# Kernel optimization log

Hardware: AMD Instinct MI355X
Metric: run time of the kernel (lower is better)

Reference implementation:

```python
import jax, jax.numpy as jnp
import numpy as np

# dims
BB, T, D_IN = 16, 2048, 64
D = 512          # hidden_dim (d_model)
DI = 2 * D       # d_inner (expand=2)
N = 16           # d_state
DC = 4           # d_conv
R = D // 16      # dt_rank = 32
L = 3            # n_layer
D_OUT = 128


def setup_inputs() -> dict:
    key = jax.random.key(0)
    ks = jax.random.split(key, 10)
    g = lambda k, shape, s: (jax.random.normal(k, shape, jnp.float32) * s)
    A_log = jnp.tile(jnp.log(jnp.arange(1, N + 1, dtype=jnp.float32))[None, None, :], (L, DI, 1))
    return {
        "x": g(ks[0], (BB, T, D_IN), 1.0),
        "Wi": g(ks[1], (D, D_IN), 0.05), "bi": jnp.zeros((D,), jnp.float32),
        "Win": g(ks[2], (L, 2 * DI, D), 0.02),
        "convw": g(ks[3], (L, DI, DC), 0.2), "convb": jnp.zeros((L, DI), jnp.float32),
        "Wx": g(ks[4], (L, R + 2 * N, DI), 0.02),
        "Wdt": g(ks[5], (L, DI, R), 0.05), "bdt": jnp.full((L, DI), -1.0, jnp.float32),
        "A_log": A_log, "Dp": jnp.ones((L, DI), jnp.float32),
        "Wout": g(ks[6], (L, D, DI), 0.02),
        "Wo": g(ks[7], (D_OUT, D), 0.05), "bo": jnp.zeros((D_OUT,), jnp.float32),
    }


def _selective_scan(u, delta, A, Bm, Cm, Dv):
    # u, delta: [B,T,DI]; A: [DI,N]; Bm, Cm: [B,T,N]; Dv: [DI]
    def step(h, inp):
        d_t, u_t, B_t, C_t = inp  # [B,DI],[B,DI],[B,N],[B,N]
        dA = jnp.exp(d_t[:, :, None] * A)                      # [B,DI,N]
        h = dA * h + (d_t * u_t)[:, :, None] * B_t[:, None, :]  # [B,DI,N]
        y = jnp.einsum('bdn,bn->bd', h, C_t)
        return h, y

    h0 = jnp.zeros((u.shape[0], u.shape[2], A.shape[1]), u.dtype)
    xs = (delta.transpose(1, 0, 2), u.transpose(1, 0, 2),
          Bm.transpose(1, 0, 2), Cm.transpose(1, 0, 2))
    _, ys = jax.lax.scan(step, h0, xs)
    return ys.transpose(1, 0, 2) + u * Dv


def _mamba_layer(x, Win, cw, cb, Wx, Wdt, bdt, A_log, Dv, Wout):
    xz = x @ Win.T                      # [B,T,2*DI]
    xin, z = jnp.split(xz, 2, axis=-1)
    # causal depthwise conv1d
    xc = jax.lax.conv_general_dilated(
        xin.transpose(0, 2, 1), cw[:, None, :], (1,), [(DC - 1, 0)],
        feature_group_count=DI, dimension_numbers=('NCH', 'OIH', 'NCH'))
    u = jax.nn.silu((xc + cb[None, :, None]).transpose(0, 2, 1))  # [B,T,DI]
    dbc = u @ Wx.T                      # [B,T,R+2N]
    dt, Bm, Cm = dbc[..., :R], dbc[..., R:R + N], dbc[..., R + N:]
    delta = jax.nn.softplus(dt @ Wdt.T + bdt)
    A = -jnp.exp(A_log)
    y = _selective_scan(u, delta, A, Bm, Cm, Dv)
    return (y * jax.nn.silu(z)) @ Wout.T


def reference(x, Wi, bi, Win, convw, convb, Wx, Wdt, bdt, A_log, Dp, Wout, Wo, bo):
    h = x @ Wi.T + bi
    for l in range(L):
        h = _mamba_layer(h, Win[l], convw[l], convb[l], Wx[l], Wdt[l], bdt[l],
                         A_log[l], Dp[l], Wout[l])
    return jnp.tanh(h @ Wo.T + bo)  # [B,T,output_dim]
```

## Files before the change

### kernel.cpp

```cpp
#include <hip/hip_runtime.h>
#include <hip/hip_bf16.h>

#define BB_ 16
#define T_ 2048
#define DIN_ 64
#define D_ 512
#define DI_ 1024
#define N_ 16
#define DC_ 4
#define R_ 32
#define L_ 3
#define DOUT_ 128
#define CL_ 64
#define NCH_ (T_ / CL_)

typedef __attribute__((ext_vector_type(8))) _Float16 f16x8;
typedef __attribute__((ext_vector_type(4))) float f32x4;

__device__ __forceinline__ float silu_f(float x) { return x / (1.f + __expf(-x)); }

__device__ __forceinline__ float softplus_f(float t) {
    return fmaxf(t, 0.f) + __logf(1.f + __expf(-fabsf(t)));
}

__device__ __forceinline__ unsigned short f2h(float f) {
    union { _Float16 h; unsigned short u; } c;
    c.h = (_Float16)f;
    return c.u;
}

__device__ __forceinline__ float h2f(unsigned short u) {
    union { unsigned short u; _Float16 h; } c;
    c.u = u;
    return (float)c.h;
}

__device__ __forceinline__ void gload_lds16(const unsigned short* g,
                                            unsigned short* l) {
    __builtin_amdgcn_global_load_lds(
        (const __attribute__((address_space(1))) void*)g,
        (__attribute__((address_space(3))) void*)l, 16, 0, 0);
}

__device__ __forceinline__ float decode_scale(unsigned int bits) {
    if (bits == 0u) return 1.f;
    const int E = (int)(bits >> 23) & 0xFF;
    return __uint_as_float((unsigned)(265 - E) << 23);
}

__device__ __forceinline__ uint4 pack8(float4 lo, float4 hi, float s) {
    union { uint4 u; unsigned short h[8]; } r;
    r.h[0] = f2h(lo.x * s); r.h[1] = f2h(lo.y * s);
    r.h[2] = f2h(lo.z * s); r.h[3] = f2h(lo.w * s);
    r.h[4] = f2h(hi.x * s); r.h[5] = f2h(hi.y * s);
    r.h[6] = f2h(hi.z * s); r.h[7] = f2h(hi.w * s);
    return r.u;
}

__device__ __forceinline__ const float* wregion(
    int r, const float* Win, const float* Wout, const float* Wx,
    const float* Wo, size_t* n4)
{
    if (r < 3)       { *n4 = 262144; return Win  + (size_t)r * 1048576; }
    else if (r < 6)  { *n4 = 131072; return Wout + (size_t)(r - 3) * 524288; }
    else if (r == 6) { *n4 = 16384;  return Wo; }
    else             { *n4 = 16384;  return Wx  + (size_t)(r - 7) * 65536; }
}

__global__ __launch_bounds__(256) void amax_all(
    const float* __restrict__ Win, const float* __restrict__ Wout,
    const float* __restrict__ Wx, const float* __restrict__ Wo,
    unsigned int* __restrict__ scales)
{
    size_t n4;
    const float* p = wregion(blockIdx.z, Win, Wout, Wx, Wo, &n4);
    float m = 0.f;
    for (size_t i = (size_t)blockIdx.x * 256 + threadIdx.x; i < n4;
         i += (size_t)gridDim.x * 256) {
        const float4 v = ((const float4*)p)[i];
        m = fmaxf(m, fmaxf(fmaxf(fabsf(v.x), fabsf(v.y)),
                           fmaxf(fabsf(v.z), fabsf(v.w))));
    }
#pragma unroll
    for (int off = 32; off; off >>= 1) m = fmaxf(m, __shfl_down(m, off));
    __shared__ float sm[4];
    if ((threadIdx.x & 63) == 0) sm[threadIdx.x >> 6] = m;
    __syncthreads();
    if (threadIdx.x == 0) {
        const float b = fmaxf(fmaxf(sm[0], sm[1]), fmaxf(sm[2], sm[3]));
        atomicMax(scales + blockIdx.z, __float_as_uint(b));
    }
}

__global__ __launch_bounds__(256) void cast_all(
    const float* __restrict__ Win, const float* __restrict__ Wout,
    const float* __restrict__ Wx, const float* __restrict__ Wo,
    unsigned short* __restrict__ WinH, unsigned short* __restrict__ WoutH,
    unsigned short* __restrict__ WxH, unsigned short* __restrict__ WoH,
    const unsigned int* __restrict__ scales)
{
    const int r = blockIdx.z;
    size_t n4;
    const float* p = wregion(r, Win, Wout, Wx, Wo, &n4);
    unsigned short* o;
    if (r < 3)       o = WinH  + (size_t)r * 1048576;
    else if (r < 6)  o = WoutH + (size_t)(r - 3) * 524288;
    else if (r == 6) o = WoH;
    else             o = WxH   + (size_t)(r - 7) * 65536;
    const float s = decode_scale(scales[r]);
    for (size_t i = (size_t)blockIdx.x * 256 + threadIdx.x; i < n4;
         i += (size_t)gridDim.x * 256) {
        const float4 v = ((const float4*)p)[i];
        ((ushort4*)o)[i] = make_ushort4(f2h(v.x * s), f2h(v.y * s),
                                        f2h(v.z * s), f2h(v.w * s));
    }
}

__global__ __launch_bounds__(256) void winrow_kernel(
    const float* __restrict__ Win, unsigned int* __restrict__ scales)
{
    const int l = blockIdx.z;
    const int row = blockIdx.x * 4 + (threadIdx.x >> 6);
    const int lane = threadIdx.x & 63;
    const float* W = Win + (size_t)l * 2 * DI_ * D_ + (size_t)row * D_ + lane * 8;
    float s = 0.f;
#pragma unroll
    for (int k = 0; k < 8; k += 4) {
        const float4 v = *(const float4*)(W + k);
        s += fabsf(v.x) + fabsf(v.y) + fabsf(v.z) + fabsf(v.w);
    }
#pragma unroll
    for (int off = 32; off; off >>= 1) s += __shfl_down(s, off);
    if (lane == 0) atomicMax(scales + 26 + l, __float_as_uint(s));
}

__global__ __launch_bounds__(256) void ubound_kernel(
    const float* __restrict__ cw, const float* __restrict__ cb,
    const unsigned int* __restrict__ hslot,
    const unsigned int* __restrict__ wbslot,
    unsigned int* __restrict__ xzbslot, unsigned int* __restrict__ uslot)
{
    const float xzb = __uint_as_float(*hslot) * __uint_as_float(*wbslot);
    if (threadIdx.x == 0) atomicMax(xzbslot, __float_as_uint(xzb));
    float m = 0.f;
    for (int c = threadIdx.x; c < DI_; c += 256) {
        const float4 w = *(const float4*)(cw + (size_t)c * 4);
        const float sw = fabsf(w.x) + fabsf(w.y) + fabsf(w.z) + fabsf(w.w);
        m = fmaxf(m, fabsf(cb[c]) + sw * xzb);
    }
#pragma unroll
    for (int off = 32; off; off >>= 1) m = fmaxf(m, __shfl_down(m, off));
    __shared__ float sm[4];
    if ((threadIdx.x & 63) == 0) sm[threadIdx.x >> 6] = m;
    __syncthreads();
    if (threadIdx.x == 0) {
        const float b = fmaxf(fmaxf(sm[0], sm[1]), fmaxf(sm[2], sm[3]));
        atomicMax(uslot, __float_as_uint(b));
    }
}

template<int ACT, int OUTH>
__global__ __launch_bounds__(256) void gemm_f32a_t128(
    const float* __restrict__ A, int lda,
    const unsigned short* __restrict__ B, int ldb,
    const float* __restrict__ bias,
    void* __restrict__ Cv, int ldc, int K,
    const unsigned int* __restrict__ sa, const unsigned int* __restrict__ sb,
    const unsigned int* __restrict__ so, unsigned int* __restrict__ oamax)
{
    __shared__ __align__(16) unsigned short As[128 * 32];
    __shared__ __align__(16) unsigned short Bs[2][128 * 32];
    const int tid  = threadIdx.x;
    const int lane = tid & 63;
    const int w    = tid >> 6;
    const int wr   = (w >> 1) << 6;
    const int wc   = (w & 1) << 6;
    const int l15  = lane & 15, l4 = lane >> 4;
    const int row0 = blockIdx.y << 7, col0 = blockIdx.x << 7;
    const int tq   = tid >> 2;
    const int tr   = (tid & 3) << 3;

    const float sA  = decode_scale(*sa);
    const float inv = (1.f / sA) * (1.f / decode_scale(*sb));
    const float sOut = OUTH ? decode_scale(*so) : 1.f;

    const float* Ar0 = A + (size_t)(row0 + tq) * lda + tr;
    const float* Ar1 = A + (size_t)(row0 + 64 + tq) * lda + tr;
    const unsigned short* Br0 = B + (size_t)(col0 + tq) * ldb + tr;
    const unsigned short* Br1 = B + (size_t)(col0 + 64 + tq) * ldb + tr;

    f32x4 acc[4][4];
#pragma unroll
    for (int m = 0; m < 4; ++m)
#pragma unroll
        for (int n = 0; n < 4; ++n) acc[m][n] = (f32x4){0.f, 0.f, 0.f, 0.f};

    float4 a0lo = *(const float4*)(Ar0), a0hi = *(const float4*)(Ar0 + 4);
    float4 a1lo = *(const float4*)(Ar1), a1hi = *(const float4*)(Ar1 + 4);
    gload_lds16(Br0, &Bs[0][tq * 32 + tr]);
    gload_lds16(Br1, &Bs[0][(64 + tq) * 32 + tr]);

    int cur = 0;
    for (int k0 = 0; k0 < K; k0 += 32) {
        __syncthreads();
        *(uint4*)&As[tq * 32 + tr]        = pack8(a0lo, a0hi, sA);
        *(uint4*)&As[(64 + tq) * 32 + tr] = pack8(a1lo, a1hi, sA);
        __syncthreads();

        if (k0 + 32 < K) {
            gload_lds16(Br0 + k0 + 32, &Bs[cur ^ 1][tq * 32 + tr]);
            gload_lds16(Br1 + k0 + 32, &Bs[cur ^ 1][(64 + tq) * 32 + tr]);
            a0lo = *(const float4*)(Ar0 + k0 + 32);
            a0hi = *(const float4*)(Ar0 + k0 + 36);
            a1lo = *(const float4*)(Ar1 + k0 + 32);
            a1hi = *(const float4*)(Ar1 + k0 + 36);
        }

        f16x8 af[4], bfr[4];
#pragma unroll
        for (int m = 0; m < 4; ++m)
            af[m] = *(const f16x8*)&As[(wr + m * 16 + l15) * 32 + l4 * 8];
#pragma unroll
        for (int n = 0; n < 4; ++n)
            bfr[n] = *(const f16x8*)&Bs[cur][(wc + n * 16 + l15) * 32 + l4 * 8];
#pragma unroll
        for (int m = 0; m < 4; ++m)
#pragma unroll
            for (int n = 0; n < 4; ++n)
                acc[m][n] = __builtin_amdgcn_mfma_f32_16x16x32_f16(
                    af[m], bfr[n], acc[m][n], 0, 0, 0);
        cur ^= 1;
    }

    float am = 0.f;
#pragma unroll
    for (int n = 0; n < 4; ++n) {
        const int col = col0 + wc + n * 16 + l15;
        float bc = 0.f;
        if (ACT == 3) bc = bias[col];
#pragma unroll
        for (int m = 0; m < 4; ++m) {
            const int rowb = row0 + wr + m * 16 + (l4 << 2);
#pragma unroll
            for (int r = 0; r < 4; ++r) {
                float v = acc[m][n][r] * inv;
                if (ACT == 3) v = tanhf(v + bc);
                if (OUTH) {
                    ((unsigned short*)Cv)[(size_t)(rowb + r) * ldc + col] =
                        f2h(v * sOut);
                } else {
                    ((float*)Cv)[(size_t)(rowb + r) * ldc + col] = v;
                    am = fmaxf(am, fabsf(v));
                }
            }
        }
    }
    if (!OUTH && oamax) {
#pragma unroll
        for (int off = 32; off; off >>= 1) am = fmaxf(am, __shfl_down(am, off));
        if (lane == 0) atomicMax(oamax, __float_as_uint(am));
    }
}

__global__ __launch_bounds__(256) void gemm_f16_t64n(
    const unsigned short* __restrict__ A, int lda,
    const unsigned short* __restrict__ B, int ldb,
    float* __restrict__ C, int ldc, int K,
    const unsigned int* __restrict__ sa, const unsigned int* __restrict__ sb)
{
    __shared__ __align__(16) unsigned short As[128 * 32];
    __shared__ __align__(16) unsigned short Bs[64 * 32];
    const int tid  = threadIdx.x;
    const int lane = tid & 63;
    const int w    = tid >> 6;
    const int l15  = lane & 15, l4 = lane >> 4;
    const int row0 = blockIdx.y << 7;
    const int tq   = tid >> 2;
    const int tr   = (tid & 3) << 3;

    const float inv = (1.f / decode_scale(*sa)) * (1.f / decode_scale(*sb));

    const unsigned short* Ar0 = A + (size_t)(row0 + tq) * lda + tr;
    const unsigned short* Ar1 = A + (size_t)(row0 + 64 + tq) * lda + tr;
    const unsigned short* Br  = B + (size_t)tq * ldb + tr;

    f32x4 acc[2][4];
#pragma unroll
    for (int m = 0; m < 2; ++m)
#pragma unroll
        for (int n = 0; n < 4; ++n) acc[m][n] = (f32x4){0.f, 0.f, 0.f, 0.f};

    uint4 av0 = *(const uint4*)(Ar0);
    uint4 av1 = *(const uint4*)(Ar1);
    uint4 bv  = *(const uint4*)(Br);

    for (int k0 = 0; k0 < K; k0 += 32) {
        __syncthreads();
        *(uint4*)&As[tq * 32 + tr]        = av0;
        *(uint4*)&As[(64 + tq) * 32 + tr] = av1;
        *(uint4*)&Bs[tq * 32 + tr]        = bv;
        __syncthreads();

        if (k0 + 32 < K) {
            av0 = *(const uint4*)(Ar0 + k0 + 32);
            av1 = *(const uint4*)(Ar1 + k0 + 32);
            bv  = *(const uint4*)(Br  + k0 + 32);
        }

        f16x8 af[2], bfr[4];
#pragma unroll
        for (int m = 0; m < 2; ++m)
            af[m] = *(const f16x8*)&As[(w * 32 + m * 16 + l15) * 32 + l4 * 8];
#pragma unroll
        for (int n = 0; n < 4; ++n)
            bfr[n] = *(const f16x8*)&Bs[(n * 16 + l15) * 32 + l4 * 8];
#pragma unroll
        for (int m = 0; m < 2; ++m)
#pragma unroll
            for (int n = 0; n < 4; ++n)
                acc[m][n] = __builtin_amdgcn_mfma_f32_16x16x32_f16(
                    af[m], bfr[n], acc[m][n], 0, 0, 0);
    }

#pragma unroll
    for (int n = 0; n < 4; ++n) {
        const int col = n * 16 + l15;
#pragma unroll
        for (int m = 0; m < 2; ++m) {
            const int rowb = row0 + w * 32 + m * 16 + (l4 << 2);
#pragma unroll
            for (int r = 0; r < 4; ++r)
                C[(size_t)(rowb + r) * ldc + col] = acc[m][n][r] * inv;
        }
    }
}

__global__ __launch_bounds__(256) void gemm_in(
    const float* __restrict__ A, int lda,
    const float* __restrict__ B, int ldb,
    const float* __restrict__ bias,
    float* __restrict__ C, int ldc, int K,
    unsigned int* __restrict__ oamax)
{
    __shared__ __align__(16) float As[8][128];
    __shared__ __align__(16) float Bs[8][128];
    const int tid  = threadIdx.x;
    const int row0 = blockIdx.y << 7;
    const int col0 = blockIdx.x << 7;
    const int tx = tid & 15, ty = tid >> 4;

    float acc[8][8];
#pragma unroll
    for (int i = 0; i < 8; ++i)
#pragma unroll
        for (int j = 0; j < 8; ++j) acc[i][j] = 0.f;

    const int arow = tid >> 1;
    const int acol = (tid & 1) << 2;
    const float* Ap = A + (size_t)(row0 + arow) * lda + acol;
    const float* Bp = B + (size_t)(col0 + arow) * ldb + acol;

    for (int k0 = 0; k0 < K; k0 += 8) {
        const float4 av = *(const float4*)(Ap + k0);
        const float4 bv = *(const float4*)(Bp + k0);
        __syncthreads();
        As[acol + 0][arow] = av.x; As[acol + 1][arow] = av.y;
        As[acol + 2][arow] = av.z; As[acol + 3][arow] = av.w;
        Bs[acol + 0][arow] = bv.x; Bs[acol + 1][arow] = bv.y;
        Bs[acol + 2][arow] = bv.z; Bs[acol + 3][arow] = bv.w;
        __syncthreads();
#pragma unroll
        for (int k = 0; k < 8; ++k) {
            float a[8], b[8];
            *(float4*)&a[0] = *(const float4*)&As[k][ty << 3];
            *(float4*)&a[4] = *(const float4*)&As[k][(ty << 3) + 4];
            *(float4*)&b[0] = *(const float4*)&Bs[k][tx << 3];
            *(float4*)&b[4] = *(const float4*)&Bs[k][(tx << 3) + 4];
#pragma unroll
            for (int i = 0; i < 8; ++i)
#pragma unroll
                for (int j = 0; j < 8; ++j)
                    acc[i][j] = fmaf(a[i], b[j], acc[i][j]);
        }
    }

    float bv8[8];
#pragma unroll
    for (int j = 0; j < 8; ++j) bv8[j] = bias[col0 + (tx << 3) + j];

    float am = 0.f;
#pragma unroll
    for (int i = 0; i < 8; ++i) {
        float v[8];
#pragma unroll
        for (int j = 0; j < 8; ++j) {
            v[j] = acc[i][j] + bv8[j];
            am = fmaxf(am, fabsf(v[j]));
        }
        float* Cp = C + (size_t)(row0 + (ty << 3) + i) * ldc + col0 + (tx << 3);
        *(float4*)(Cp)     = make_float4(v[0], v[1], v[2], v[3]);
        *(float4*)(Cp + 4) = make_float4(v[4], v[5], v[6], v[7]);
    }
#pragma unroll
    for (int off = 32; off; off >>= 1) am = fmaxf(am, __shfl_down(am, off));
    if ((tid & 63) == 0) atomicMax(oamax, __float_as_uint(am));
}

__global__ __launch_bounds__(256) void conv_silu_kernel(
    const unsigned short* __restrict__ xzh, const float* __restrict__ cw,
    const float* __restrict__ cb, unsigned short* __restrict__ u,
    size_t total4, const unsigned int* __restrict__ xzbslot,
    const unsigned int* __restrict__ uslot)
{
    const float invX = 1.f / decode_scale(*xzbslot);
    const float s = decode_scale(*uslot);
    for (size_t i = (size_t)blockIdx.x * 256 + threadIdx.x; i < total4;
         i += (size_t)gridDim.x * 256) {
        const size_t e = i * 4;
        const int c = (int)(e & (DI_ - 1));
        const size_t m = e >> 10;
        const int t = (int)(m & (T_ - 1));
        const unsigned short* xr = xzh + m * 2048 + c;
        float x[4][4];
#pragma unroll
        for (int k = 0; k < 4; ++k) {
            const int dt = 3 - k;
            if (t >= dt) {
                const ushort4 xv = *(const ushort4*)(xr - (size_t)dt * 2048);
                x[k][0] = h2f(xv.x) * invX; x[k][1] = h2f(xv.y) * invX;
                x[k][2] = h2f(xv.z) * invX; x[k][3] = h2f(xv.w) * invX;
            } else {
                x[k][0] = x[k][1] = x[k][2] = x[k][3] = 0.f;
            }
        }
        const float4 cbv = *(const float4*)(cb + c);
        ushort4 o;
        {
            const float4 w = *(const float4*)(cw + (size_t)c * 4);
            o.x = f2h(silu_f(fmaf(x[3][0], w.w, fmaf(x[2][0], w.z,
                     fmaf(x[1][0], w.y, fmaf(x[0][0], w.x, cbv.x))))) * s);
        }
        {
            const float4 w = *(const float4*)(cw + (size_t)(c + 1) * 4);
            o.y = f2h(silu_f(fmaf(x[3][1], w.w, fmaf(x[2][1], w.z,
                     fmaf(x[1][1], w.y, fmaf(x[0][1], w.x, cbv.y))))) * s);
        }
        {
            const float4 w = *(const float4*)(cw + (size_t)(c + 2) * 4);
            o.z = f2h(silu_f(fmaf(x[3][2], w.w, fmaf(x[2][2], w.z,
                     fmaf(x[1][2], w.y, fmaf(x[0][2], w.x, cbv.z))))) * s);
        }
        {
            const float4 w = *(const float4*)(cw + (size_t)(c + 3) * 4);
            o.w = f2h(silu_f(fmaf(x[3][3], w.w, fmaf(x[2][3], w.z,
                     fmaf(x[1][3], w.y, fmaf(x[0][3], w.x, cbv.w))))) * s);
        }
        *(ushort4*)(u + e) = o;
    }
}


__device__ __forceinline__ bool geo_check(const float* a2) {
    bool ok = true;
#pragma unroll
    for (int n = 1; n < N_; ++n)
        ok = ok && (fabsf(a2[n] - a2[0] * (n + 1)) <=
                    1e-5f * fmaxf(1.f, fabsf(a2[n])));
    return ok;
}

__global__ __launch_bounds__(256) void scan_pass1(
    const unsigned short* __restrict__ u, const float* __restrict__ dbc,
    const float* __restrict__ A_log_l, const float* __restrict__ Wdt_l,
    const float* __restrict__ bdt_l, const unsigned int* __restrict__ uslot,
    float* __restrict__ SDL, float* __restrict__ S)
{
    __shared__ __align__(16) float sAll[CL_][64];
    const int tid = threadIdx.x;
    const int b = blockIdx.x, ch = blockIdx.z;
    const int d = (blockIdx.y << 8) + tid;

    float a2[N_], hs[N_];
#pragma unroll
    for (int n = 0; n < N_; ++n) {
        a2[n] = -__expf(A_log_l[d * N_ + n]) * 1.44269504f;
        hs[n] = 0.f;
    }
    const bool geo = geo_check(a2);
    const float invU = 1.f / decode_scale(*uslot);
    float wdt[32];
#pragma unroll
    for (int k = 0; k < 32; k += 4)
        *(float4*)&wdt[k] = *(const float4*)(Wdt_l + (size_t)d * 32 + k);
    const float bdt_d = bdt_l[d];

    const size_t base64 = ((size_t)b * T_ + (size_t)ch * CL_) * 64;
    float* sflat = &sAll[0][0];
    for (int i = tid; i < CL_ * 64; i += 256) sflat[i] = dbc[base64 + i];
    __syncthreads();

    float sdl = 0.f;
    if (geo) {
        for (int tt = 0; tt < CL_; ++tt) {
            float t = bdt_d;
#pragma unroll
            for (int k = 0; k < 32; k += 4) {
                const float4 dv = *(const float4*)&sAll[tt][k];
                t = fmaf(dv.x, wdt[k + 0], t);
                t = fmaf(dv.y, wdt[k + 1], t);
                t = fmaf(dv.z, wdt[k + 2], t);
                t = fmaf(dv.w, wdt[k + 3], t);
            }
            const float dl = softplus_f(t);
            sdl += dl;
            const size_t m = (size_t)b * T_ + ch * CL_ + tt;
            const float du = dl * (h2f(u[m * DI_ + d]) * invU);
            const float r = exp2f(dl * a2[0]);
            float dA = r;
#pragma unroll
            for (int n = 0; n < N_; ++n) {
                hs[n] = fmaf(dA, hs[n], du * sAll[tt][32 + n]);
                dA *= r;
            }
        }
    } else {
        for (int tt = 0; tt < CL_; ++tt) {
            float t = bdt_d;
#pragma unroll
            for (int k = 0; k < 32; k += 4) {
                const float4 dv = *(const float4*)&sAll[tt][k];
                t = fmaf(dv.x, wdt[k + 0], t);
                t = fmaf(dv.y, wdt[k + 1], t);
                t = fmaf(dv.z, wdt[k + 2], t);
                t = fmaf(dv.w, wdt[k + 3], t);
            }
            const float dl = softplus_f(t);
            sdl += dl;
            const size_t m = (size_t)b * T_ + ch * CL_ + tt;
            const float du = dl * (h2f(u[m * DI_ + d]) * invU);
#pragma unroll
            for (int n = 0; n < N_; ++n) {
                const float dA = exp2f(dl * a2[n]);
                hs[n] = fmaf(dA, hs[n], du * sAll[tt][32 + n]);
            }
        }
    }
    SDL[(size_t)((b * NCH_ + ch) << 10) + d] = sdl;
#pragma unroll
    for (int n = 0; n < N_; ++n) {
        const size_t idx = (size_t)(((b * NCH_ + ch) * N_ + n) << 10) + d;
        S[idx] = hs[n];
    }
}

__global__ __launch_bounds__(256) void scan_carry(
    const float* __restrict__ SDL, float* __restrict__ S,
    const float* __restrict__ A_log_l)
{
    const size_t gid = (size_t)blockIdx.x * 256 + threadIdx.x;
    const int d = (int)(gid & 1023);
    const int n = (int)((gid >> 10) & 15);
    const int b = (int)(gid >> 14);
    const float a2n = -__expf(A_log_l[d * N_ + n]) * 1.44269504f;
    float hc = 0.f;
    for (int ch = 0; ch < NCH_; ++ch) {
        const float sdl = SDL[(size_t)((b * NCH_ + ch) << 10) + d];
        const float p = exp2f(sdl * a2n);
        const size_t idx = (size_t)(((b * NCH_ + ch) * N_ + n) << 10) + d;
        const float s = S[idx];
        S[idx] = hc;
        hc = fmaf(p, hc, s);
    }
}

__global__ __launch_bounds__(256) void scan_pass3(
    const unsigned short* __restrict__ xzh, float* __restrict__ g,
    const unsigned short* __restrict__ u, const float* __restrict__ dbc,
    const float* __restrict__ A_log_l, const float* __restrict__ Wdt_l,
    const float* __restrict__ bdt_l, const float* __restrict__ Dp_l,
    const unsigned int* __restrict__ xzbslot,
    const unsigned int* __restrict__ uslot,
    const float* __restrict__ S, unsigned int* __restrict__ gmax)
{
    __shared__ __align__(16) float sAll[CL_][64];
    const int tid = threadIdx.x;
    const int b = blockIdx.x, ch = blockIdx.z;
    const int d = (blockIdx.y << 8) + tid;

    float a2[N_], hs[N_];
#pragma unroll
    for (int n = 0; n < N_; ++n) {
        a2[n] = -__expf(A_log_l[d * N_ + n]) * 1.44269504f;
        hs[n] = S[(size_t)(((b * NCH_ + ch) * N_ + n) << 10) + d];
    }
    const bool geo = geo_check(a2);
    const float invX = 1.f / decode_scale(*xzbslot);
    const float invU = 1.f / decode_scale(*uslot);
    float wdt[32];
#pragma unroll
    for (int k = 0; k < 32; k += 4)
        *(float4*)&wdt[k] = *(const float4*)(Wdt_l + (size_t)d * 32 + k);
    const float bdt_d = bdt_l[d];
    const float Dpd = Dp_l[d];

    const size_t base64 = ((size_t)b * T_ + (size_t)ch * CL_) * 64;
    float* sflat = &sAll[0][0];
    for (int i = tid; i < CL_ * 64; i += 256) sflat[i] = dbc[base64 + i];
    __syncthreads();

    float gm = 0.f;
    if (geo) {
        for (int tt = 0; tt < CL_; ++tt) {
            float t = bdt_d;
#pragma unroll
            for (int k = 0; k < 32; k += 4) {
                const float4 dv = *(const float4*)&sAll[tt][k];
                t = fmaf(dv.x, wdt[k + 0], t);
                t = fmaf(dv.y, wdt[k + 1], t);
                t = fmaf(dv.z, wdt[k + 2], t);
                t = fmaf(dv.w, wdt[k + 3], t);
            }
            const float dl = softplus_f(t);
            const size_t m = (size_t)b * T_ + ch * CL_ + tt;
            const float uv = h2f(u[m * DI_ + d]) * invU;
            const float du = dl * uv;
            const float r = exp2f(dl * a2[0]);
            float dA = r;
            float yv = 0.f;
#pragma unroll
            for (int n = 0; n < N_; ++n) {
                hs[n] = fmaf(dA, hs[n], du * sAll[tt][32 + n]);
                yv = fmaf(hs[n], sAll[tt][48 + n], yv);
                dA *= r;
            }
            yv = fmaf(uv, Dpd, yv);
            const float zv = h2f(xzh[m * 2048 + DI_ + d]) * invX;
            const float gv = yv * silu_f(zv);
            g[m * DI_ + d] = gv;
            gm = fmaxf(gm, fabsf(gv));
        }
    } else {
        for (int tt = 0; tt < CL_; ++tt) {
            float t = bdt_d;
#pragma unroll
            for (int k = 0; k < 32; k += 4) {
                const float4 dv = *(const float4*)&sAll[tt][k];
                t = fmaf(dv.x, wdt[k + 0], t);
                t = fmaf(dv.y, wdt[k + 1], t);
                t = fmaf(dv.z, wdt[k + 2], t);
                t = fmaf(dv.w, wdt[k + 3], t);
            }
            const float dl = softplus_f(t);
            const size_t m = (size_t)b * T_ + ch * CL_ + tt;
            const float uv = h2f(u[m * DI_ + d]) * invU;
            const float du = dl * uv;
            float yv = 0.f;
#pragma unroll
            for (int n = 0; n < N_; ++n) {
                const float dA = exp2f(dl * a2[n]);
                hs[n] = fmaf(dA, hs[n], du * sAll[tt][32 + n]);
                yv = fmaf(hs[n], sAll[tt][48 + n], yv);
            }
            yv = fmaf(uv, Dpd, yv);
            const float zv = h2f(xzh[m * 2048 + DI_ + d]) * invX;
            const float gv = yv * silu_f(zv);
            g[m * DI_ + d] = gv;
            gm = fmaxf(gm, fabsf(gv));
        }
    }
#pragma unroll
    for (int off = 32; off; off >>= 1) gm = fmaxf(gm, __shfl_down(gm, off));
    if ((tid & 63) == 0) atomicMax(gmax, __float_as_uint(gm));
}

extern "C" void kernel_launch(void* const* d_in, const int* in_sizes, int n_in,
                              void* d_out, int out_size, void* d_ws, size_t ws_size,
                              hipStream_t stream) {
    const float* x     = (const float*)d_in[0];
    const float* Wi    = (const float*)d_in[1];
    const float* bi    = (const float*)d_in[2];
    const float* Win   = (const float*)d_in[3];
    const float* convw = (const float*)d_in[4];
    const float* convb = (const float*)d_in[5];
    const float* Wx    = (const float*)d_in[6];
    const float* Wdt   = (const float*)d_in[7];
    const float* bdt   = (const float*)d_in[8];
    const float* A_log = (const float*)d_in[9];
    const float* Dp    = (const float*)d_in[10];
    const float* Wout  = (const float*)d_in[11];
    const float* Wo    = (const float*)d_in[12];
    const float* bo    = (const float*)d_in[13];
    float* out = (float*)d_out;

    const size_t rowf = 3648;
    const size_t wextra =
        (3 * 1048576 + 3 * 524288 + 65536 + 3 * 65536) / 2 + 32;
    int CB = BB_;
    while (CB > 1 && ((size_t)CB * T_ * rowf + wextra) * sizeof(float) > ws_size) CB >>= 1;
    const size_t Mc = (size_t)CB * T_;

    const dim3 blk(256);
    const int rowTiles = (int)(Mc / 128);

    float* ws   = (float*)d_ws;
    unsigned short* xzh = (unsigned short*)ws;
    float* gbuf = ws + Mc * 1024;
    unsigned short* ub = (unsigned short*)(gbuf + Mc * 1024);
    float* dbc  = gbuf + Mc * 1024 + Mc * 512;
    float* hPS  = dbc + Mc * 64;
    float* hb   = hPS;
    float* Sdl  = hPS;
    float* Sbuf = hPS + Mc * 16;
    unsigned short* WinH  = (unsigned short*)(hPS + Mc * 512);
    unsigned short* WoutH = WinH + 3 * 1048576;
    unsigned short* WoH   = WoutH + 3 * 524288;
    unsigned short* WxH   = WoH + 65536;
    unsigned int* scales  = (unsigned int*)(WxH + 3 * 65536);

    hipMemsetAsync(scales, 0, 32 * sizeof(unsigned int), stream);

    amax_all<<<dim3(128, 1, 10), blk, 0, stream>>>(Win, Wout, Wx, Wo, scales);
    winrow_kernel<<<dim3(512, 1, 3), blk, 0, stream>>>(Win, scales);
    cast_all<<<dim3(64, 1, 10), blk, 0, stream>>>(
        Win, Wout, Wx, Wo, WinH, WoutH, WxH, WoH, scales);

    for (int c = 0; c < BB_ / CB; ++c) {
        const float* x_c = x + (size_t)c * Mc * DIN_;
        float* out_c     = out + (size_t)c * Mc * DOUT_;

        hipMemsetAsync(scales + 10, 0, 16 * sizeof(unsigned int), stream);

        gemm_in<<<dim3(D_ / 128, rowTiles), blk, 0, stream>>>(
            x_c, DIN_, Wi, DIN_, bi, hb, D_, DIN_, scales + 10);

        for (int l = 0; l < L_; ++l) {
            const float* cw_l   = convw + (size_t)l * DI_ * DC_;
            const float* cb_l   = convb + (size_t)l * DI_;
            const float* Wdt_l  = Wdt  + (size_t)l * DI_ * R_;
            const float* bdt_l  = bdt  + (size_t)l * DI_;
            const float* Alog_l = A_log + (size_t)l * DI_ * N_;
            const float* Dp_l   = Dp   + (size_t)l * DI_;

            ubound_kernel<<<dim3(1), blk, 0, stream>>>(
                cw_l, cb_l, scales + 10 + l, scales + 26 + l,
                scales + 17 + l, scales + 20 + l);

            gemm_f32a_t128<0, 1><<<dim3(2048 / 128, rowTiles), blk, 0, stream>>>(
                hb, D_, WinH + (size_t)l * 1048576, D_, nullptr,
                xzh, 2048, D_, scales + 10 + l, scales + l,
                scales + 17 + l, nullptr);

            conv_silu_kernel<<<dim3(2048), blk, 0, stream>>>(
                xzh, cw_l, cb_l, ub, Mc * DI_ / 4,
                scales + 17 + l, scales + 20 + l);

            gemm_f16_t64n<<<dim3(1, rowTiles), blk, 0, stream>>>(
                ub, DI_, WxH + (size_t)l * 65536, DI_, dbc, 64, DI_,
                scales + 20 + l, scales + 7 + l);

            scan_pass1<<<dim3(CB, DI_ / 256, NCH_), blk, 0, stream>>>(
                ub, dbc, Alog_l, Wdt_l, bdt_l, scales + 20 + l, Sdl, Sbuf);
            scan_carry<<<dim3(CB * 64), blk, 0, stream>>>(Sdl, Sbuf, Alog_l);
            scan_pass3<<<dim3(CB, DI_ / 256, NCH_), blk, 0, stream>>>(
                xzh, gbuf, ub, dbc, Alog_l, Wdt_l, bdt_l, Dp_l,
                scales + 17 + l, scales + 20 + l, Sbuf, scales + 14 + l);

            gemm_f32a_t128<0, 0><<<dim3(D_ / 128, rowTiles), blk, 0, stream>>>(
                gbuf, DI_, WoutH + (size_t)l * 524288, DI_, nullptr,
                hb, D_, DI_, scales + 14 + l, scales + 3 + l,
                nullptr, scales + 11 + l);
        }

        gemm_f32a_t128<3, 0><<<dim3(DOUT_ / 128, rowTiles), blk, 0, stream>>>(
            hb, D_, WoH, D_, bo, out_c, DOUT_, D_,
            scales + 13, scales + 6, nullptr, nullptr);
    }
}
```

Baseline: 2.182 ms.

## Store delta in fp16 from scan pass1 and reuse it in pass3

Scan pass1 now writes the softplus delta as fp16 to a new buffer, and pass3 reads it instead of recomputing the 32-term dt projection and softplus. Pass3 stages only the B/C columns in shared memory. The chunk length is halved, which doubles the number of chunks and the length of the carry sequence. Chunk states are stored as fp16 to offset the larger state buffer. This trades recomputation for an extra 2-byte-per-element write and read, and adds fp16 rounding on delta and on the carried states.

```diff
diff --git a/kernel.cpp b/kernel.cpp
--- a/kernel.cpp
+++ b/kernel.cpp
@@ -11,7 +11,7 @@
 #define R_ 32
 #define L_ 3
 #define DOUT_ 128
-#define CL_ 64
+#define CL_ 32
 #define NCH_ (T_ / CL_)
 
 typedef __attribute__((ext_vector_type(8))) _Float16 f16x8;
@@ -473,7 +473,8 @@
     const unsigned short* __restrict__ u, const float* __restrict__ dbc,
     const float* __restrict__ A_log_l, const float* __restrict__ Wdt_l,
     const float* __restrict__ bdt_l, const unsigned int* __restrict__ uslot,
-    float* __restrict__ SDL, float* __restrict__ S)
+    unsigned short* __restrict__ dlh,
+    float* __restrict__ SDL, unsigned short* __restrict__ S16)
 {
     __shared__ __align__(16) float sAll[CL_][64];
     const int tid = threadIdx.x;
@@ -500,21 +501,22 @@
     __syncthreads();
 
     float sdl = 0.f;
-    if (geo) {
-        for (int tt = 0; tt < CL_; ++tt) {
-            float t = bdt_d;
-#pragma unroll
-            for (int k = 0; k < 32; k += 4) {
-                const float4 dv = *(const float4*)&sAll[tt][k];
-                t = fmaf(dv.x, wdt[k + 0], t);
-                t = fmaf(dv.y, wdt[k + 1], t);
-                t = fmaf(dv.z, wdt[k + 2], t);
-                t = fmaf(dv.w, wdt[k + 3], t);
-            }
-            const float dl = softplus_f(t);
-            sdl += dl;
-            const size_t m = (size_t)b * T_ + ch * CL_ + tt;
-            const float du = dl * (h2f(u[m * DI_ + d]) * invU);
+    for (int tt = 0; tt < CL_; ++tt) {
+        float t = bdt_d;
+#pragma unroll
+        for (int k = 0; k < 32; k += 4) {
+            const float4 dv = *(const float4*)&sAll[tt][k];
+            t = fmaf(dv.x, wdt[k + 0], t);
+            t = fmaf(dv.y, wdt[k + 1], t);
+            t = fmaf(dv.z, wdt[k + 2], t);
+            t = fmaf(dv.w, wdt[k + 3], t);
+        }
+        const float dl = softplus_f(t);
+        sdl += dl;
+        const size_t m = (size_t)b * T_ + ch * CL_ + tt;
+        dlh[m * DI_ + d] = f2h(dl);
+        const float du = dl * (h2f(u[m * DI_ + d]) * invU);
+        if (geo) {
             const float r = exp2f(dl * a2[0]);
             float dA = r;
 #pragma unroll
@@ -522,22 +524,7 @@
                 hs[n] = fmaf(dA, hs[n], du * sAll[tt][32 + n]);
                 dA *= r;
             }
-        }
-    } else {
-        for (int tt = 0; tt < CL_; ++tt) {
-            float t = bdt_d;
-#pragma unroll
-            for (int k = 0; k < 32; k += 4) {
-                const float4 dv = *(const float4*)&sAll[tt][k];
-                t = fmaf(dv.x, wdt[k + 0], t);
-                t = fmaf(dv.y, wdt[k + 1], t);
-                t = fmaf(dv.z, wdt[k + 2], t);
-                t = fmaf(dv.w, wdt[k + 3], t);
-            }
-            const float dl = softplus_f(t);
-            sdl += dl;
-            const size_t m = (size_t)b * T_ + ch * CL_ + tt;
-            const float du = dl * (h2f(u[m * DI_ + d]) * invU);
+        } else {
 #pragma unroll
             for (int n = 0; n < N_; ++n) {
                 const float dA = exp2f(dl * a2[n]);
@@ -549,12 +536,12 @@
 #pragma unroll
     for (int n = 0; n < N_; ++n) {
         const size_t idx = (size_t)(((b * NCH_ + ch) * N_ + n) << 10) + d;
-        S[idx] = hs[n];
+        S16[idx] = f2h(hs[n]);
     }
 }
 
 __global__ __launch_bounds__(256) void scan_carry(
-    const float* __restrict__ SDL, float* __restrict__ S,
+    const float* __restrict__ SDL, unsigned short* __restrict__ S16,
     const float* __restrict__ A_log_l)
 {
     const size_t gid = (size_t)blockIdx.x * 256 + threadIdx.x;
@@ -567,22 +554,23 @@
         const float sdl = SDL[(size_t)((b * NCH_ + ch) << 10) + d];
         const float p = exp2f(sdl * a2n);
         const size_t idx = (size_t)(((b * NCH_ + ch) * N_ + n) << 10) + d;
-        const float s = S[idx];
-        S[idx] = hc;
+        const float s = h2f(S16[idx]);
+        S16[idx] = f2h(hc);
         hc = fmaf(p, hc, s);
     }
 }
 
 __global__ __launch_bounds__(256) void scan_pass3(
     const unsigned short* __restrict__ xzh, float* __restrict__ g,
-    const unsigned short* __restrict__ u, const float* __restrict__ dbc,
-    const float* __restrict__ A_log_l, const float* __restrict__ Wdt_l,
-    const float* __restrict__ bdt_l, const float* __restrict__ Dp_l,
+    const unsigned short* __restrict__ u,
+    const unsigned short* __restrict__ dlh,
+    const float* __restrict__ dbc, const float* __restrict__ A_log_l,
+    const float* __restrict__ Dp_l,
     const unsigned int* __restrict__ xzbslot,
     const unsigned int* __restrict__ uslot,
-    const float* __restrict__ S, unsigned int* __restrict__ gmax)
-{
-    __shared__ __align__(16) float sAll[CL_][64];
+    const unsigned short* __restrict__ S16, unsigned int* __restrict__ gmax)
+{
+    __shared__ __align__(16) float sBC[CL_][32];
     const int tid = threadIdx.x;
     const int b = blockIdx.x, ch = blockIdx.z;
     const int d = (blockIdx.y << 8) + tid;
@@ -591,82 +579,49 @@
 #pragma unroll
     for (int n = 0; n < N_; ++n) {
         a2[n] = -__expf(A_log_l[d * N_ + n]) * 1.44269504f;
-        hs[n] = S[(size_t)(((b * NCH_ + ch) * N_ + n) << 10) + d];
+        hs[n] = h2f(S16[(size_t)(((b * NCH_ + ch) * N_ + n) << 10) + d]);
     }
     const bool geo = geo_check(a2);
     const float invX = 1.f / decode_scale(*xzbslot);
     const float invU = 1.f / decode_scale(*uslot);
-    float wdt[32];
-#pragma unroll
-    for (int k = 0; k < 32; k += 4)
-        *(float4*)&wdt[k] = *(const float4*)(Wdt_l + (size_t)d * 32 + k);
-    const float bdt_d = bdt_l[d];
     const float Dpd = Dp_l[d];
 
     const size_t base64 = ((size_t)b * T_ + (size_t)ch * CL_) * 64;
-    float* sflat = &sAll[0][0];
-    for (int i = tid; i < CL_ * 64; i += 256) sflat[i] = dbc[base64 + i];
+    for (int i = tid; i < CL_ * 32; i += 256) {
+        const int row = i >> 5, col = i & 31;
+        sBC[row][col] = dbc[base64 + (size_t)row * 64 + 32 + col];
+    }
     __syncthreads();
 
     float gm = 0.f;
-    if (geo) {
-        for (int tt = 0; tt < CL_; ++tt) {
-            float t = bdt_d;
-#pragma unroll
-            for (int k = 0; k < 32; k += 4) {
-                const float4 dv = *(const float4*)&sAll[tt][k];
-                t = fmaf(dv.x, wdt[k + 0], t);
-                t = fmaf(dv.y, wdt[k + 1], t);
-                t = fmaf(dv.z, wdt[k + 2], t);
-                t = fmaf(dv.w, wdt[k + 3], t);
-            }
-            const float dl = softplus_f(t);
-            const size_t m = (size_t)b * T_ + ch * CL_ + tt;
-            const float uv = h2f(u[m * DI_ + d]) * invU;
-            const float du = dl * uv;
+    for (int tt = 0; tt < CL_; ++tt) {
+        const size_t m = (size_t)b * T_ + ch * CL_ + tt;
+        const float dl = h2f(dlh[m * DI_ + d]);
+        const float uv = h2f(u[m * DI_ + d]) * invU;
+        const float du = dl * uv;
+        float yv = 0.f;
+        if (geo) {
             const float r = exp2f(dl * a2[0]);
             float dA = r;
-            float yv = 0.f;
 #pragma unroll
             for (int n = 0; n < N_; ++n) {
-                hs[n] = fmaf(dA, hs[n], du * sAll[tt][32 + n]);
-                yv = fmaf(hs[n], sAll[tt][48 + n], yv);
+                hs[n] = fmaf(dA, hs[n], du * sBC[tt][n]);
+                yv = fmaf(hs[n], sBC[tt][16 + n], yv);
                 dA *= r;
             }
-            yv = fmaf(uv, Dpd, yv);
-            const float zv = h2f(xzh[m * 2048 + DI_ + d]) * invX;
-            const float gv = yv * silu_f(zv);
-            g[m * DI_ + d] = gv;
-            gm = fmaxf(gm, fabsf(gv));
-        }
-    } else {
-        for (int tt = 0; tt < CL_; ++tt) {
-            float t = bdt_d;
-#pragma unroll
-            for (int k = 0; k < 32; k += 4) {
-                const float4 dv = *(const float4*)&sAll[tt][k];
-                t = fmaf(dv.x, wdt[k + 0], t);
-                t = fmaf(dv.y, wdt[k + 1], t);
-                t = fmaf(dv.z, wdt[k + 2], t);
-                t = fmaf(dv.w, wdt[k + 3], t);
-            }
-            const float dl = softplus_f(t);
-            const size_t m = (size_t)b * T_ + ch * CL_ + tt;
-            const float uv = h2f(u[m * DI_ + d]) * invU;
-            const float du = dl * uv;
-            float yv = 0.f;
+        } else {
 #pragma unroll
             for (int n = 0; n < N_; ++n) {
                 const float dA = exp2f(dl * a2[n]);
-                hs[n] = fmaf(dA, hs[n], du * sAll[tt][32 + n]);
-                yv = fmaf(hs[n], sAll[tt][48 + n], yv);
+                hs[n] = fmaf(dA, hs[n], du * sBC[tt][n]);
+                yv = fmaf(hs[n], sBC[tt][16 + n], yv);
             }
-            yv = fmaf(uv, Dpd, yv);
-            const float zv = h2f(xzh[m * 2048 + DI_ + d]) * invX;
-            const float gv = yv * silu_f(zv);
-            g[m * DI_ + d] = gv;
-            gm = fmaxf(gm, fabsf(gv));
-        }
+        }
+        yv = fmaf(uv, Dpd, yv);
+        const float zv = h2f(xzh[m * 2048 + DI_ + d]) * invX;
+        const float gv = yv * silu_f(zv);
+        g[m * DI_ + d] = gv;
+        gm = fmaxf(gm, fabsf(gv));
     }
 #pragma unroll
     for (int off = 32; off; off >>= 1) gm = fmaxf(gm, __shfl_down(gm, off));
@@ -706,11 +661,12 @@
     unsigned short* xzh = (unsigned short*)ws;
     float* gbuf = ws + Mc * 1024;
     unsigned short* ub = (unsigned short*)(gbuf + Mc * 1024);
-    float* dbc  = gbuf + Mc * 1024 + Mc * 512;
+    unsigned short* dlh = ub + Mc * 1024;
+    float* dbc  = gbuf + Mc * 1024 + Mc * 1024;
     float* hPS  = dbc + Mc * 64;
     float* hb   = hPS;
     float* Sdl  = hPS;
-    float* Sbuf = hPS + Mc * 16;
+    unsigned short* S16 = (unsigned short*)(hPS + Mc * 32);
     unsigned short* WinH  = (unsigned short*)(hPS + Mc * 512);
     unsigned short* WoutH = WinH + 3 * 1048576;
     unsigned short* WoH   = WoutH + 3 * 524288;
@@ -759,11 +715,12 @@
                 scales + 20 + l, scales + 7 + l);
 
             scan_pass1<<<dim3(CB, DI_ / 256, NCH_), blk, 0, stream>>>(
-                ub, dbc, Alog_l, Wdt_l, bdt_l, scales + 20 + l, Sdl, Sbuf);
-            scan_carry<<<dim3(CB * 64), blk, 0, stream>>>(Sdl, Sbuf, Alog_l);
+                ub, dbc, Alog_l, Wdt_l, bdt_l, scales + 20 + l,
+                dlh, Sdl, S16);
+            scan_carry<<<dim3(CB * 64), blk, 0, stream>>>(Sdl, S16, Alog_l);
             scan_pass3<<<dim3(CB, DI_ / 256, NCH_), blk, 0, stream>>>(
-                xzh, gbuf, ub, dbc, Alog_l, Wdt_l, bdt_l, Dp_l,
-                scales + 17 + l, scales + 20 + l, Sbuf, scales + 14 + l);
+                xzh, gbuf, ub, dlh, dbc, Alog_l, Dp_l,
+                scales + 17 + l, scales + 20 + l, S16, scales + 14 + l);
 
             gemm_f32a_t128<0, 0><<<dim3(D_ / 128, rowTiles), blk, 0, stream>>>(
                 gbuf, DI_, WoutH + (size_t)l * 524288, DI_, nullptr,
```

New measurement: 2.559 ms. 1.17x slower.
